# Kernel tuning notes

Measured on AMD Instinct MI355X. Metric: run time of the kernel, lower is better.

## Reference

```python
import jax, jax.numpy as jnp
import numpy as np

B, T, D, H = 2, 2048, 1024, 16
HD = D // H
SCALE = HD ** -0.5


def setup_inputs() -> dict:
    key = jax.random.key(0)
    k1, k2, k3 = jax.random.split(key, 3)
    x = jax.random.normal(k1, (B, T, D), dtype=jnp.float32)
    w_qkv = jax.random.normal(k2, (D, 3 * D), dtype=jnp.float32) * (D ** -0.5)
    w_proj = jax.random.normal(k3, (D, D), dtype=jnp.float32) * (D ** -0.5)
    b_proj = jnp.zeros((D,), dtype=jnp.float32)
    return {"x": x, "w_qkv": w_qkv, "w_proj": w_proj, "b_proj": b_proj}


def reference(x, w_qkv, w_proj, b_proj):
    b, t, d = x.shape
    qkv = jnp.einsum('btd,de->bte', x, w_qkv)            # [B,T,3D]
    qkv = qkv.reshape(b, t, 3, H, HD)
    q = qkv[:, :, 0].transpose(0, 2, 1, 3)               # [B,H,T,HD]
    k = qkv[:, :, 1].transpose(0, 2, 1, 3)
    v = qkv[:, :, 2].transpose(0, 2, 1, 3)
    scores = jnp.einsum('bhqd,bhkd->bhqk', q, k) * SCALE  # [B,H,T,T]
    # NOTE: faithful to the source, softmax over dim=1 (the HEAD axis)
    probs = jax.nn.softmax(scores, axis=1)
    attn_out = jnp.einsum('bhqk,bhkd->bhqd', probs, v)
    attn_out = attn_out.transpose(0, 2, 1, 3).reshape(b, t, d)
    out = jnp.einsum('btd,de->bte', attn_out, w_proj) + b_proj
    return out
```

## Files before the change

kernel.cpp:

```cpp
#include <hip/hip_runtime.h>
#include <hip/hip_bf16.h>
#include <stdint.h>

typedef __bf16 bf16;
typedef __attribute__((ext_vector_type(8))) __bf16 bf16x8;
typedef __attribute__((ext_vector_type(4))) __bf16 bf16x4;
typedef __attribute__((ext_vector_type(2))) __bf16 bf16x2;
typedef __attribute__((ext_vector_type(4))) float f32x4;

#define MFMA_16x16x32(a, b, c) __builtin_amdgcn_mfma_f32_16x16x32_bf16((a), (b), (c), 0, 0, 0)

__device__ __forceinline__ void gld_lds16(const void* g, void* l) {
    __builtin_amdgcn_global_load_lds(
        (const __attribute__((address_space(1))) void*)g,
        (__attribute__((address_space(3))) void*)l,
        16, 0, 0);
}

__global__ void cvt_f32_bf16(const float* __restrict__ in, bf16* __restrict__ out, int n) {
    int i = (blockIdx.x * blockDim.x + threadIdx.x) * 8;
    if (i >= n) return;
    f32x4 a = *(const f32x4*)(in + i);
    f32x4 b = *(const f32x4*)(in + i + 4);
    bf16x8 o;
#pragma unroll
    for (int j = 0; j < 4; ++j) { o[j] = (bf16)a[j]; o[j + 4] = (bf16)b[j]; }
    *(bf16x8*)(out + i) = o;
}

__global__ void transpose_cvt(const float* __restrict__ in, bf16* __restrict__ out, int R, int C) {
    __shared__ float tile[32][33];
    int c0 = blockIdx.x * 32, r0 = blockIdx.y * 32;
    int tc = threadIdx.x & 31, tr = threadIdx.x >> 5;
#pragma unroll
    for (int i = 0; i < 4; ++i) {
        int r = tr + i * 8;
        tile[r][tc] = in[(size_t)(r0 + r) * C + c0 + tc];
    }
    __syncthreads();
#pragma unroll
    for (int i = 0; i < 4; ++i) {
        int r = tr + i * 8;
        out[(size_t)(c0 + r) * R + r0 + tc] = (bf16)tile[tc][r];
    }
}

template <int EPI>
__global__ void __launch_bounds__(256) gemm_bf16(
    const bf16* __restrict__ A, const bf16* __restrict__ Bt, int M, int N, int K,
    float* __restrict__ Cf, const float* __restrict__ bias,
    bf16* __restrict__ q_out, bf16* __restrict__ k_out, bf16* __restrict__ v_out)
{
    __shared__ bf16 As[128 * 32];
    __shared__ bf16 Bs[128 * 32];
    const int t = threadIdx.x, w = t >> 6, l = t & 63;
    const int l15 = l & 15, lh = l >> 4;
    const int m0 = blockIdx.y * 128, n0 = blockIdx.x * 128;
    const int wm = w >> 1, wn = w & 1;

    const int srow = w * 16 + (l >> 2);
    const int scol = (l & 3) * 8;
    const bf16* gA = A + (size_t)(m0 + srow) * K + scol;
    const bf16* gB = Bt + (size_t)(n0 + srow) * K + scol;
    char* lA = (char*)As + w * 1024;
    char* lB = (char*)Bs + w * 1024;

    f32x4 acc[4][4] = {};

    for (int kt = 0; kt < K; kt += 32) {
        __syncthreads();
        gld_lds16(gA + kt, lA);
        gld_lds16(gA + (size_t)64 * K + kt, lA + 4096);
        gld_lds16(gB + kt, lB);
        gld_lds16(gB + (size_t)64 * K + kt, lB + 4096);
        asm volatile("s_waitcnt vmcnt(0)" ::: "memory");
        __syncthreads();

        const bf16* pa = As + (wm * 64 + l15) * 32 + lh * 8;
        const bf16* pb = Bs + (wn * 64 + l15) * 32 + lh * 8;
        bf16x8 af[4], bfr[4];
#pragma unroll
        for (int i = 0; i < 4; ++i) {
            af[i]  = *(const bf16x8*)(pa + i * 512);
            bfr[i] = *(const bf16x8*)(pb + i * 512);
        }
#pragma unroll
        for (int mi = 0; mi < 4; ++mi)
#pragma unroll
            for (int ni = 0; ni < 4; ++ni)
                acc[mi][ni] = MFMA_16x16x32(af[mi], bfr[ni], acc[mi][ni]);
    }

    if (EPI == 1) {
#pragma unroll
        for (int ni = 0; ni < 4; ++ni) {
            int n = n0 + wn * 64 + ni * 16 + l15;
            float bb = bias[n];
#pragma unroll
            for (int mi = 0; mi < 4; ++mi)
#pragma unroll
                for (int r = 0; r < 4; ++r) {
                    int m = m0 + wm * 64 + mi * 16 + lh * 4 + r;
                    Cf[(size_t)m * N + n] = acc[mi][ni][r] + bb;
                }
        }
    } else {
        const int which = n0 >> 10;
        const float QSCL = 0.125f * 1.44269504089f;
#pragma unroll
        for (int ni = 0; ni < 4; ++ni) {
            int n = n0 + wn * 64 + ni * 16 + l15;
            int h = (n >> 6) & 15;
            int d = n & 63;
#pragma unroll
            for (int mi = 0; mi < 4; ++mi)
#pragma unroll
                for (int r = 0; r < 4; ++r) {
                    int m = m0 + wm * 64 + mi * 16 + lh * 4 + r;
                    int b = m >> 11, tt = m & 2047;
                    float av = acc[mi][ni][r];
                    size_t hb = (size_t)b * 16 + h;
                    if (which == 0)      q_out[(hb * 2048 + tt) * 64 + d] = (bf16)(av * QSCL);
                    else if (which == 1) k_out[(hb * 2048 + tt) * 64 + d] = (bf16)av;
                    else                 v_out[(hb * 64 + d) * 2048 + tt] = (bf16)av;
                }
        }
    }
}

__global__ void __launch_bounds__(1024, 4) attn_kernel(
    const bf16* __restrict__ Q, const bf16* __restrict__ Kmat, const bf16* __restrict__ Vt,
    bf16* __restrict__ p0, bf16* __restrict__ p1, bf16* __restrict__ p2, bf16* __restrict__ p3)
{
    __shared__ bf16 S[2][16][32][72];
    const int t = threadIdx.x;
    const int w = t >> 6;
    const int l = t & 63;
    const int l15 = l & 15, lh = l >> 4;

    const int bid = blockIdx.x;
    const int b = (bid & 7) >> 2;
    const int ks = bid & 3;
    const int qt = (bid >> 3) * 32;

    const size_t headQK = ((size_t)b * 16 + w) * (2048 * 64);
    const size_t headV  = ((size_t)b * 16 + w) * (64 * 2048);

    bf16x8 qf[2][2];
#pragma unroll
    for (int qb2 = 0; qb2 < 2; ++qb2)
#pragma unroll
        for (int dc = 0; dc < 2; ++dc)
            qf[qb2][dc] = *(const bf16x8*)(Q + headQK + (size_t)(qt + qb2 * 16 + l15) * 64 + dc * 32 + lh * 8);

    f32x4 o[2][4] = {};

    auto SCORE = [&](int g, int buf) {
        const int kt = ks * 512 + g * 64;
#pragma unroll
        for (int kb = 0; kb < 4; ++kb) {
            const bf16* kp = Kmat + headQK + (size_t)(kt + kb * 16 + l15) * 64 + lh * 8;
            bf16x8 ak0 = *(const bf16x8*)(kp);
            bf16x8 ak1 = *(const bf16x8*)(kp + 32);
#pragma unroll
            for (int qb2 = 0; qb2 < 2; ++qb2) {
                f32x4 s = {};
                s = MFMA_16x16x32(ak0, qf[qb2][0], s);
                s = MFMA_16x16x32(ak1, qf[qb2][1], s);
                bf16x4 pk;
#pragma unroll
                for (int r = 0; r < 4; ++r)
                    pk[r] = (bf16)__builtin_amdgcn_exp2f(s[r]);
                *(bf16x4*)&S[buf][w][qb2 * 16 + l15][kb * 16 + lh * 4] = pk;
            }
        }
    };
    auto SUMNORM = [&](int buf) {
        const int sq = t >> 5, kc = (t & 31) * 2;
        float e0[16], e1[16];
        float s0 = 0.f, s1 = 0.f;
#pragma unroll
        for (int hh = 0; hh < 16; ++hh) {
            bf16x2 pr = *(const bf16x2*)&S[buf][hh][sq][kc];
            e0[hh] = (float)pr[0]; e1[hh] = (float)pr[1];
            s0 += e0[hh]; s1 += e1[hh];
        }
        float iv0 = __builtin_amdgcn_rcpf(s0);
        float iv1 = __builtin_amdgcn_rcpf(s1);
#pragma unroll
        for (int hh = 0; hh < 16; ++hh) {
            bf16x2 pv;
            pv[0] = (bf16)(e0[hh] * iv0);
            pv[1] = (bf16)(e1[hh] * iv1);
            *(bf16x2*)&S[buf][hh][sq][kc] = pv;
        }
    };
    auto PV = [&](int g, int buf) {
        const int kt = ks * 512 + g * 64;
#pragma unroll
        for (int ksub = 0; ksub < 2; ++ksub) {
            bf16x8 bv[4];
#pragma unroll
            for (int ni = 0; ni < 4; ++ni)
                bv[ni] = *(const bf16x8*)(Vt + headV + (size_t)(ni * 16 + l15) * 2048 + kt + ksub * 32 + lh * 8);
#pragma unroll
            for (int qb2 = 0; qb2 < 2; ++qb2) {
                bf16x8 ap = *(const bf16x8*)(&S[buf][w][qb2 * 16 + l15][ksub * 32 + lh * 8]);
#pragma unroll
                for (int ni = 0; ni < 4; ++ni)
                    o[qb2][ni] = MFMA_16x16x32(ap, bv[ni], o[qb2][ni]);
            }
        }
    };

    SCORE(0, 0);
    __syncthreads();
    SUMNORM(0);
    __syncthreads();
    for (int g = 1; g < 8; ++g) {
        PV(g - 1, (g - 1) & 1);
        SCORE(g, g & 1);
        __syncthreads();
        SUMNORM(g & 1);
        __syncthreads();
    }
    PV(7, 1);

    bf16* dst = (ks == 0 ? p0 : ks == 1 ? p1 : ks == 2 ? p2 : p3) + (size_t)b * (2048 * 1024);
#pragma unroll
    for (int qb2 = 0; qb2 < 2; ++qb2)
#pragma unroll
        for (int ni = 0; ni < 4; ++ni)
#pragma unroll
            for (int r = 0; r < 4; ++r) {
                int tt = qt + qb2 * 16 + lh * 4 + r;
                int d = ni * 16 + l15;
                dst[(size_t)tt * 1024 + w * 64 + d] = (bf16)o[qb2][ni][r];
            }
}

__global__ void reduce_part4(const bf16* __restrict__ p0, const bf16* __restrict__ p1,
                             const bf16* __restrict__ p2, const bf16* __restrict__ p3,
                             bf16* __restrict__ out, int n) {
    int i = (blockIdx.x * blockDim.x + threadIdx.x) * 8;
    if (i >= n) return;
    bf16x8 a = *(const bf16x8*)(p0 + i);
    bf16x8 b = *(const bf16x8*)(p1 + i);
    bf16x8 c = *(const bf16x8*)(p2 + i);
    bf16x8 d = *(const bf16x8*)(p3 + i);
    bf16x8 o;
#pragma unroll
    for (int j = 0; j < 8; ++j)
        o[j] = (bf16)(((float)a[j] + (float)b[j]) + ((float)c[j] + (float)d[j]));
    *(bf16x8*)(out + i) = o;
}

extern "C" void kernel_launch(void* const* d_in, const int* in_sizes, int n_in,
                              void* d_out, int out_size, void* d_ws, size_t ws_size,
                              hipStream_t stream)
{
    const float* x      = (const float*)d_in[0];
    const float* w_qkv  = (const float*)d_in[1];
    const float* w_proj = (const float*)d_in[2];
    const float* b_proj = (const float*)d_in[3];
    float* out = (float*)d_out;

    char* ws = (char*)d_ws;
    const size_t MB = 1048576;
    bf16* wprojT = (bf16*)(ws + 0 * MB);
    bf16* xb     = (bf16*)(ws + 2 * MB);
    bf16* wqkvT  = (bf16*)(ws + 10 * MB);
    bf16* qb     = (bf16*)(ws + 18 * MB);
    bf16* kb     = (bf16*)(ws + 26 * MB);
    bf16* vt     = (bf16*)(ws + 34 * MB);
    bf16* part0  = (bf16*)(ws + 2 * MB);
    bf16* part1  = (bf16*)(ws + 10 * MB);
    bf16* part2  = (bf16*)(ws + 42 * MB);
    bf16* part3  = (bf16*)(ws + 50 * MB);
    bf16* attnb  = (bf16*)(ws + 2 * MB);

    cvt_f32_bf16<<<2048, 256, 0, stream>>>(x, xb, 4194304);
    transpose_cvt<<<dim3(96, 32), 256, 0, stream>>>(w_qkv, wqkvT, 1024, 3072);
    transpose_cvt<<<dim3(32, 32), 256, 0, stream>>>(w_proj, wprojT, 1024, 1024);

    gemm_bf16<0><<<dim3(24, 32), 256, 0, stream>>>(xb, wqkvT, 4096, 3072, 1024,
                                                   nullptr, nullptr, qb, kb, vt);
    attn_kernel<<<512, 1024, 0, stream>>>(qb, kb, vt, part0, part1, part2, part3);
    reduce_part4<<<2048, 256, 0, stream>>>(part0, part1, part2, part3, attnb, 4194304);
    gemm_bf16<1><<<dim3(8, 32), 256, 0, stream>>>(attnb, wprojT, 4096, 1024, 1024,
                                                  out, b_proj, nullptr, nullptr, nullptr);

    (void)in_sizes; (void)n_in; (void)out_size; (void)ws_size;
}
```

Measured before the change: 238.4 us.

## Prefetch K tiles one step ahead and issue V loads before barriers in attention loop

Splits the K and V global loads out of the score and PV stages into separate register-prefetch helpers. K for the next tile is loaded into a double-buffered register set while the current tile is scored, and V is loaded before the barrier and softmax-normalise phase so its latency is hidden. The loop is fully unrolled and PV now runs after the normalise step of the same iteration rather than overlapping with the next score. SUMNORM re-reads LDS instead of holding 32 floats in registers, trading extra LDS reads for lower register pressure, which the additional prefetch registers may need.

```diff
diff --git a/kernel.cpp b/kernel.cpp
--- a/kernel.cpp
+++ b/kernel.cpp
@@ -155,18 +155,31 @@
 
     f32x4 o[2][4] = {};
 
-    auto SCORE = [&](int g, int buf) {
+    auto loadK = [&](int g, bf16x8 (&kf)[4][2]) {
         const int kt = ks * 512 + g * 64;
 #pragma unroll
         for (int kb = 0; kb < 4; ++kb) {
             const bf16* kp = Kmat + headQK + (size_t)(kt + kb * 16 + l15) * 64 + lh * 8;
-            bf16x8 ak0 = *(const bf16x8*)(kp);
-            bf16x8 ak1 = *(const bf16x8*)(kp + 32);
+            kf[kb][0] = *(const bf16x8*)(kp);
+            kf[kb][1] = *(const bf16x8*)(kp + 32);
+        }
+    };
+    auto loadV = [&](int g, bf16x8 (&vf)[2][4]) {
+        const int kt = ks * 512 + g * 64;
+#pragma unroll
+        for (int ksub = 0; ksub < 2; ++ksub)
+#pragma unroll
+            for (int ni = 0; ni < 4; ++ni)
+                vf[ksub][ni] = *(const bf16x8*)(Vt + headV + (size_t)(ni * 16 + l15) * 2048 + kt + ksub * 32 + lh * 8);
+    };
+    auto SCORE = [&](bf16x8 (&kf)[4][2], int buf) {
+#pragma unroll
+        for (int kb = 0; kb < 4; ++kb) {
 #pragma unroll
             for (int qb2 = 0; qb2 < 2; ++qb2) {
                 f32x4 s = {};
-                s = MFMA_16x16x32(ak0, qf[qb2][0], s);
-                s = MFMA_16x16x32(ak1, qf[qb2][1], s);
+                s = MFMA_16x16x32(kf[kb][0], qf[qb2][0], s);
+                s = MFMA_16x16x32(kf[kb][1], qf[qb2][1], s);
                 bf16x4 pk;
 #pragma unroll
                 for (int r = 0; r < 4; ++r)
@@ -177,54 +190,50 @@
     };
     auto SUMNORM = [&](int buf) {
         const int sq = t >> 5, kc = (t & 31) * 2;
-        float e0[16], e1[16];
         float s0 = 0.f, s1 = 0.f;
 #pragma unroll
         for (int hh = 0; hh < 16; ++hh) {
             bf16x2 pr = *(const bf16x2*)&S[buf][hh][sq][kc];
-            e0[hh] = (float)pr[0]; e1[hh] = (float)pr[1];
-            s0 += e0[hh]; s1 += e1[hh];
+            s0 += (float)pr[0]; s1 += (float)pr[1];
         }
         float iv0 = __builtin_amdgcn_rcpf(s0);
         float iv1 = __builtin_amdgcn_rcpf(s1);
 #pragma unroll
         for (int hh = 0; hh < 16; ++hh) {
+            bf16x2 pr = *(const bf16x2*)&S[buf][hh][sq][kc];
             bf16x2 pv;
-            pv[0] = (bf16)(e0[hh] * iv0);
-            pv[1] = (bf16)(e1[hh] * iv1);
+            pv[0] = (bf16)((float)pr[0] * iv0);
+            pv[1] = (bf16)((float)pr[1] * iv1);
             *(bf16x2*)&S[buf][hh][sq][kc] = pv;
         }
     };
-    auto PV = [&](int g, int buf) {
-        const int kt = ks * 512 + g * 64;
-#pragma unroll
-        for (int ksub = 0; ksub < 2; ++ksub) {
-            bf16x8 bv[4];
-#pragma unroll
-            for (int ni = 0; ni < 4; ++ni)
-                bv[ni] = *(const bf16x8*)(Vt + headV + (size_t)(ni * 16 + l15) * 2048 + kt + ksub * 32 + lh * 8);
+    auto PV = [&](bf16x8 (&vf)[2][4], int buf) {
+#pragma unroll
+        for (int ksub = 0; ksub < 2; ++ksub)
 #pragma unroll
             for (int qb2 = 0; qb2 < 2; ++qb2) {
                 bf16x8 ap = *(const bf16x8*)(&S[buf][w][qb2 * 16 + l15][ksub * 32 + lh * 8]);
 #pragma unroll
                 for (int ni = 0; ni < 4; ++ni)
-                    o[qb2][ni] = MFMA_16x16x32(ap, bv[ni], o[qb2][ni]);
+                    o[qb2][ni] = MFMA_16x16x32(ap, vf[ksub][ni], o[qb2][ni]);
             }
-        }
-    };
-
-    SCORE(0, 0);
-    __syncthreads();
-    SUMNORM(0);
-    __syncthreads();
-    for (int g = 1; g < 8; ++g) {
-        PV(g - 1, (g - 1) & 1);
-        SCORE(g, g & 1);
+    };
+
+    bf16x8 kfA[4][2], kfB[4][2], vf[2][4];
+    loadK(0, kfA);
+#pragma unroll
+    for (int g = 0; g < 8; ++g) {
+        const int buf = g & 1;
+        loadV(g, vf);
+        if (g & 1) SCORE(kfB, buf); else SCORE(kfA, buf);
+        if (g < 7) {
+            if (g & 1) loadK(g + 1, kfA); else loadK(g + 1, kfB);
+        }
         __syncthreads();
-        SUMNORM(g & 1);
+        SUMNORM(buf);
         __syncthreads();
-    }
-    PV(7, 1);
+        PV(vf, buf);
+    }
 
     bf16* dst = (ks == 0 ? p0 : ks == 1 ? p1 : ks == 2 ? p2 : p3) + (size_t)b * (2048 * 1024);
 #pragma unroll
```

Result: slower. 366.9 us (+53.9%).

## Defer cross-head softmax normalization into PV and use lightweight barriers

Applied to the files above, without the earlier changes.

The sum pass now writes only per-position reciprocals to a small shared buffer instead of rewriting all 16 heads' probabilities. Each wave multiplies its exp values by the reciprocals just before the PV MFMAs, which removes most LDS write traffic and the per-thread e0/e1 register arrays. __syncthreads is replaced by a barrier that waits only on LDS counters, so global K/V loads can stay in flight across it. The change also raises wave priority around the MFMA bursts and fully unrolls the group loop. In exchange, PV does an extra LDS read and eight multiplies per fragment, and the bf16 reciprocal adds a second rounding step.

```diff
diff --git a/kernel.cpp b/kernel.cpp
--- a/kernel.cpp
+++ b/kernel.cpp
@@ -133,6 +133,7 @@
     bf16* __restrict__ p0, bf16* __restrict__ p1, bf16* __restrict__ p2, bf16* __restrict__ p3)
 {
     __shared__ bf16 S[2][16][32][72];
+    __shared__ bf16 invS[32][72];
     const int t = threadIdx.x;
     const int w = t >> 6;
     const int l = t & 63;
@@ -154,6 +155,10 @@
             qf[qb2][dc] = *(const bf16x8*)(Q + headQK + (size_t)(qt + qb2 * 16 + l15) * 64 + dc * 32 + lh * 8);
 
     f32x4 o[2][4] = {};
+
+#define RAW_BARRIER() do { asm volatile("s_waitcnt lgkmcnt(0)" ::: "memory"); \
+                           __builtin_amdgcn_s_barrier(); \
+                           __builtin_amdgcn_sched_barrier(0); } while (0)
 
     auto SCORE = [&](int g, int buf) {
         const int kt = ks * 512 + g * 64;
@@ -175,25 +180,18 @@
             }
         }
     };
-    auto SUMNORM = [&](int buf) {
+    auto SUM = [&](int buf) {
         const int sq = t >> 5, kc = (t & 31) * 2;
-        float e0[16], e1[16];
         float s0 = 0.f, s1 = 0.f;
 #pragma unroll
         for (int hh = 0; hh < 16; ++hh) {
             bf16x2 pr = *(const bf16x2*)&S[buf][hh][sq][kc];
-            e0[hh] = (float)pr[0]; e1[hh] = (float)pr[1];
-            s0 += e0[hh]; s1 += e1[hh];
-        }
-        float iv0 = __builtin_amdgcn_rcpf(s0);
-        float iv1 = __builtin_amdgcn_rcpf(s1);
-#pragma unroll
-        for (int hh = 0; hh < 16; ++hh) {
-            bf16x2 pv;
-            pv[0] = (bf16)(e0[hh] * iv0);
-            pv[1] = (bf16)(e1[hh] * iv1);
-            *(bf16x2*)&S[buf][hh][sq][kc] = pv;
-        }
+            s0 += (float)pr[0]; s1 += (float)pr[1];
+        }
+        bf16x2 iv;
+        iv[0] = (bf16)__builtin_amdgcn_rcpf(s0);
+        iv[1] = (bf16)__builtin_amdgcn_rcpf(s1);
+        *(bf16x2*)&invS[sq][kc] = iv;
     };
     auto PV = [&](int g, int buf) {
         const int kt = ks * 512 + g * 64;
@@ -205,26 +203,36 @@
                 bv[ni] = *(const bf16x8*)(Vt + headV + (size_t)(ni * 16 + l15) * 2048 + kt + ksub * 32 + lh * 8);
 #pragma unroll
             for (int qb2 = 0; qb2 < 2; ++qb2) {
-                bf16x8 ap = *(const bf16x8*)(&S[buf][w][qb2 * 16 + l15][ksub * 32 + lh * 8]);
+                bf16x8 ev  = *(const bf16x8*)(&S[buf][w][qb2 * 16 + l15][ksub * 32 + lh * 8]);
+                bf16x8 ivv = *(const bf16x8*)(&invS[qb2 * 16 + l15][ksub * 32 + lh * 8]);
+                bf16x8 ap;
+#pragma unroll
+                for (int j = 0; j < 8; ++j)
+                    ap[j] = (bf16)((float)ev[j] * (float)ivv[j]);
+                __builtin_amdgcn_s_setprio(1);
 #pragma unroll
                 for (int ni = 0; ni < 4; ++ni)
                     o[qb2][ni] = MFMA_16x16x32(ap, bv[ni], o[qb2][ni]);
+                __builtin_amdgcn_s_setprio(0);
             }
         }
     };
 
     SCORE(0, 0);
-    __syncthreads();
-    SUMNORM(0);
-    __syncthreads();
+    RAW_BARRIER();
+    SUM(0);
+    RAW_BARRIER();
+#pragma unroll
     for (int g = 1; g < 8; ++g) {
         PV(g - 1, (g - 1) & 1);
         SCORE(g, g & 1);
-        __syncthreads();
-        SUMNORM(g & 1);
-        __syncthreads();
+        RAW_BARRIER();
+        SUM(g & 1);
+        RAW_BARRIER();
     }
     PV(7, 1);
+
+#undef RAW_BARRIER
 
     bf16* dst = (ks == 0 ? p0 : ks == 1 ? p1 : ks == 2 ? p2 : p3) + (size_t)b * (2048 * 1024);
 #pragma unroll
```

Result: faster. 231.2 us (-3.0%).
